# Optimization experiments

Hardware: AMD Instinct MI355X
Metric: run time of the kernel (lower is better)

The kernel has to match this reference:

```python
import jax, jax.numpy as jnp
import numpy as np

D_STATE = 8
DT_RANK = 16
D_CONV = 4


def layernorm(x, w, b, eps=1e-5):
    mu = jnp.mean(x, axis=-1, keepdims=True)
    var = jnp.var(x, axis=-1, keepdims=True)
    return (x - mu) * jax.lax.rsqrt(var + eps) * w + b


def silu(x):
    return x * jax.nn.sigmoid(x)


def dwconv_causal(x, w, b):
    # x: [B,L,D], w: [D,K] depthwise causal conv (mamba conv1d, padding=K-1 then truncate)
    K = w.shape[1]
    xp = jnp.pad(x, ((0, 0), (K - 1, 0), (0, 0)))
    y = jax.lax.conv_general_dilated(
        xp, w.T[:, None, :], (1,), 'VALID',
        dimension_numbers=('NWC', 'WIO', 'NWC'),
        feature_group_count=w.shape[0])
    return y + b


def selective_scan(u, dt, A, Bm, Cm, Dp):
    # u, dt: [b,l,d]; A: [d,n]; Bm, Cm: [b,l,n]; Dp: [d]
    def step(h, inp):
        dt_t, B_t, C_t, u_t = inp           # [b,d],[b,n],[b,n],[b,d]
        dA = jnp.exp(dt_t[..., None] * A)   # [b,d,n]
        h = dA * h + dt_t[..., None] * B_t[:, None, :] * u_t[..., None]
        y = jnp.einsum('bdn,bn->bd', h, C_t)
        return h, y
    b, l, d = u.shape
    h0 = jnp.zeros((b, d, A.shape[1]), u.dtype)
    xs = (dt.transpose(1, 0, 2), Bm.transpose(1, 0, 2),
          Cm.transpose(1, 0, 2), u.transpose(1, 0, 2))
    _, ys = jax.lax.scan(step, h0, xs)
    return ys.transpose(1, 0, 2) + u * Dp


def scan_dir(x, xe, cw, cb, cew, ceb, xpw, dtw, dtb, A_log, Dp):
    # one scan direction: u from x (input0 path), dt/B/C from xe (extra_emb path)
    xc = silu(dwconv_causal(x, cw, cb))
    ec = silu(dwconv_causal(xe, cew, ceb))
    dbl = ec @ xpw.T                                   # [b,l,dt_rank+2n]
    dtr = dbl[..., :DT_RANK]
    Bm = dbl[..., DT_RANK:DT_RANK + D_STATE]
    Cm = dbl[..., DT_RANK + D_STATE:]
    dt = jax.nn.softplus(dtr @ dtw.T + dtb)
    A = -jnp.exp(A_log)
    return selective_scan(xc, dt, A, Bm, Cm, Dp)


def forward(input0, input1, norm0_w, norm0_b, norm1_w, norm1_b,
            in_proj_w, in_proj_extra_w,
            convx_w, convx_b, conve_w, conve_b,
            convx_w_r, convx_b_r, conve_w_r, conve_b_r,
            xproj_w, xproj_w_r, dtproj_w, dtproj_b, dtproj_w_r, dtproj_b_r,
            A_log, A_log_r, Dp, Dp_r, outnorm_w, outnorm_b, outproj_w):
    skip = input0
    h0 = layernorm(input0, norm0_w, norm0_b)
    h1 = layernorm(input1, norm1_w, norm1_b)
    xz = h0 @ in_proj_w.T                     # [b,l,2d]
    d = in_proj_w.shape[0] // 2
    x, z = xz[..., :d], xz[..., d:]
    xe = h1 @ in_proj_extra_w.T               # [b,l,d]
    # forward-direction scan
    y_f = scan_dir(x, xe, convx_w, convx_b, conve_w, conve_b,
                   xproj_w, dtproj_w, dtproj_b, A_log, Dp)
    # backward-direction scan (flip sequence, scan, flip back)
    xr, xer = jnp.flip(x, 1), jnp.flip(xe, 1)
    y_b = scan_dir(xr, xer, convx_w_r, convx_b_r, conve_w_r, conve_b_r,
                   xproj_w_r, dtproj_w_r, dtproj_b_r, A_log_r, Dp_r)
    y = (y_f + jnp.flip(y_b, 1)) * 0.5        # if_devide_out=True
    y = layernorm(y, outnorm_w, outnorm_b)    # use_norm=True
    y = y * silu(z)
    out = y @ outproj_w.T
    return out + skip


def setup_inputs() -> dict:
    key = jax.random.key(0)
    B, H, W, dim = 2, 128, 128, 256
    L, d, n, dtr, K = H * W, dim, D_STATE, DT_RANK, D_CONV
    ks = jax.random.split(key, 24)
    s = 0.02
    inp = {
        'input0': jax.random.normal(ks[0], (B, L, dim), jnp.float32),
        'input1': jax.random.normal(ks[1], (B, L, dim), jnp.float32),
        'norm0_w': jnp.ones((dim,), jnp.float32),
        'norm0_b': jnp.zeros((dim,), jnp.float32),
        'norm1_w': jnp.ones((dim,), jnp.float32),
        'norm1_b': jnp.zeros((dim,), jnp.float32),
        'in_proj_w': jax.random.normal(ks[2], (2 * d, dim), jnp.float32) * s,
        'in_proj_extra_w': jax.random.normal(ks[3], (d, dim), jnp.float32) * s,
        'convx_w': jax.random.normal(ks[4], (d, K), jnp.float32) * 0.2,
        'convx_b': jnp.zeros((d,), jnp.float32),
        'conve_w': jax.random.normal(ks[5], (d, K), jnp.float32) * 0.2,
        'conve_b': jnp.zeros((d,), jnp.float32),
        'convx_w_r': jax.random.normal(ks[6], (d, K), jnp.float32) * 0.2,
        'convx_b_r': jnp.zeros((d,), jnp.float32),
        'conve_w_r': jax.random.normal(ks[7], (d, K), jnp.float32) * 0.2,
        'conve_b_r': jnp.zeros((d,), jnp.float32),
        'xproj_w': jax.random.normal(ks[8], (dtr + 2 * n, d), jnp.float32) * s,
        'xproj_w_r': jax.random.normal(ks[9], (dtr + 2 * n, d), jnp.float32) * s,
        'dtproj_w': jax.random.normal(ks[10], (d, dtr), jnp.float32) * 0.1,
        'dtproj_b': jax.random.uniform(ks[11], (d,), jnp.float32, -4.0, -2.0),
        'dtproj_w_r': jax.random.normal(ks[12], (d, dtr), jnp.float32) * 0.1,
        'dtproj_b_r': jax.random.uniform(ks[13], (d,), jnp.float32, -4.0, -2.0),
        'A_log': jnp.tile(jnp.log(jnp.arange(1, n + 1, dtype=jnp.float32)), (d, 1)),
        'A_log_r': jnp.tile(jnp.log(jnp.arange(1, n + 1, dtype=jnp.float32)), (d, 1)),
        'Dp': jnp.ones((d,), jnp.float32),
        'Dp_r': jnp.ones((d,), jnp.float32),
        'outnorm_w': jnp.ones((d,), jnp.float32),
        'outnorm_b': jnp.zeros((d,), jnp.float32),
        'outproj_w': jax.random.normal(ks[14], (dim, d), jnp.float32) * s,
    }
    return inp


def reference(input0, input1, norm0_w, norm0_b, norm1_w, norm1_b,
              in_proj_w, in_proj_extra_w,
              convx_w, convx_b, conve_w, conve_b,
              convx_w_r, convx_b_r, conve_w_r, conve_b_r,
              xproj_w, xproj_w_r, dtproj_w, dtproj_b, dtproj_w_r, dtproj_b_r,
              A_log, A_log_r, Dp, Dp_r, outnorm_w, outnorm_b, outproj_w):
    return forward(input0, input1, norm0_w, norm0_b, norm1_w, norm1_b,
                   in_proj_w, in_proj_extra_w,
                   convx_w, convx_b, conve_w, conve_b,
                   convx_w_r, convx_b_r, conve_w_r, conve_b_r,
                   xproj_w, xproj_w_r, dtproj_w, dtproj_b, dtproj_w_r, dtproj_b_r,
                   A_log, A_log_r, Dp, Dp_r, outnorm_w, outnorm_b, outproj_w)
```

## Files before the change

kernel.cpp:

```cpp
#include <hip/hip_runtime.h>
#include <math.h>

#define L_SEQ 16384
#define DIM 256
#define NST 8
#define RNK 16
#define S_TOT 32768
#define NCH 512
#define CLH 32

typedef __attribute__((ext_vector_type(8))) short bf16x8;
typedef __attribute__((ext_vector_type(4))) float f32x4;

__device__ __forceinline__ float bf2f(unsigned short u) {
  union { unsigned int i; float f; } v; v.i = ((unsigned int)u) << 16; return v.f;
}
__device__ __forceinline__ unsigned short f2bf(float x) {
  union { float f; unsigned int i; } v; v.f = x;
  unsigned int r = v.i + 0x7fffu + ((v.i >> 16) & 1u);
  return (unsigned short)(r >> 16);
}
__device__ __forceinline__ float rcpf(float x) {
  return __builtin_amdgcn_rcpf(x);
}

__global__ __launch_bounds__(256) void ln_norm(
    const float* __restrict__ in0, const float* __restrict__ in1,
    const float* __restrict__ w0, const float* __restrict__ b0,
    const float* __restrict__ w1, const float* __restrict__ b1,
    unsigned short* __restrict__ h0, unsigned short* __restrict__ h1,
    const float* __restrict__ pw0, const float* __restrict__ pw1,
    const float* __restrict__ pw2, unsigned short* __restrict__ wbout) {
  int which = blockIdx.y;
  if (which == 0 && blockIdx.x < 1024) {
    int i = blockIdx.x * 256 + threadIdx.x;
    if (i < 131072) wbout[i] = f2bf(pw0[i]);
    else if (i < 196608) wbout[i] = f2bf(pw1[i - 131072]);
    else wbout[i] = f2bf(pw2[i - 196608]);
  }
  int row = blockIdx.x * 4 + (threadIdx.x >> 6);
  int lane = threadIdx.x & 63;
  const float* x = (which ? in1 : in0) + (size_t)row * DIM;
  const float* w = which ? w1 : w0;
  const float* b = which ? b1 : b0;
  unsigned short* h = which ? h1 : h0;
  float4 v = *(const float4*)&x[lane * 4];
  float s = v.x + v.y + v.z + v.w;
  float s2 = v.x * v.x + v.y * v.y + v.z * v.z + v.w * v.w;
  for (int off = 32; off; off >>= 1) {
    s += __shfl_xor(s, off);
    s2 += __shfl_xor(s2, off);
  }
  float mean = s * (1.0f / DIM);
  float var = s2 * (1.0f / DIM) - mean * mean;
  float rstd = rsqrtf(var + 1e-5f);
  float4 wv = *(const float4*)&w[lane * 4];
  float4 bv = *(const float4*)&b[lane * 4];
  ushort4 out;
  out.x = f2bf((v.x - mean) * rstd * wv.x + bv.x);
  out.y = f2bf((v.y - mean) * rstd * wv.y + bv.y);
  out.z = f2bf((v.z - mean) * rstd * wv.z + bv.z);
  out.w = f2bf((v.w - mean) * rstd * wv.w + bv.w);
  *(ushort4*)&h[(size_t)row * DIM + lane * 4] = out;
}

template <int BF16C, int ADDIN>
__global__ __launch_bounds__(256) void gemm64(
    const unsigned short* __restrict__ A, int lda,
    const unsigned short* __restrict__ Wb,
    void* __restrict__ Cv, const float* __restrict__ addp, int Nn) {
  __shared__ unsigned short As[64 * 256];
  __shared__ unsigned short Ws[64 * 256];
  int tid = threadIdx.x;
  int n0 = blockIdx.x * 64, m0 = blockIdx.y * 64;
  for (int i = 0; i < 8; ++i) {
    int f8 = tid + i * 256;
    int r = f8 >> 5, c8 = (f8 & 31) * 8;
    int sc = c8 ^ ((r & 7) << 3);
    *(uint4*)&As[r * 256 + sc] = *(const uint4*)&A[(size_t)(m0 + r) * lda + c8];
    *(uint4*)&Ws[r * 256 + sc] = *(const uint4*)&Wb[(size_t)(n0 + r) * 256 + c8];
  }
  __syncthreads();
  int wid = tid >> 6, lane = tid & 63;
  int wm = wid >> 1, wn = wid & 1;
  int l15 = lane & 15, lk = (lane >> 4) * 8;
  f32x4 acc[2][2] = {};
  for (int ks = 0; ks < 8; ++ks) {
    int kcol = ks * 32 + lk;
    bf16x8 af[2], bf_[2];
    for (int mf = 0; mf < 2; ++mf) {
      int row = wm * 32 + mf * 16 + l15;
      af[mf] = *(const bf16x8*)&As[row * 256 + (kcol ^ ((row & 7) << 3))];
    }
    for (int nf = 0; nf < 2; ++nf) {
      int row = wn * 32 + nf * 16 + l15;
      bf_[nf] = *(const bf16x8*)&Ws[row * 256 + (kcol ^ ((row & 7) << 3))];
    }
    for (int mf = 0; mf < 2; ++mf)
      for (int nf = 0; nf < 2; ++nf)
        acc[mf][nf] = __builtin_amdgcn_mfma_f32_16x16x32_bf16(
            af[mf], bf_[nf], acc[mf][nf], 0, 0, 0);
  }
  for (int mf = 0; mf < 2; ++mf)
    for (int nf = 0; nf < 2; ++nf) {
      int row = m0 + wm * 32 + mf * 16 + (lane >> 4) * 4;
      int col = n0 + wn * 32 + nf * 16 + l15;
      for (int v = 0; v < 4; ++v) {
        size_t off = (size_t)(row + v) * Nn + col;
        float val = acc[mf][nf][v];
        if (ADDIN) val += addp[off];
        if (BF16C) ((unsigned short*)Cv)[off] = f2bf(val);
        else       ((float*)Cv)[off] = val;
      }
    }
}

__global__ __launch_bounds__(256) void gemm_in(
    const unsigned short* __restrict__ h0, const unsigned short* __restrict__ h1,
    const unsigned short* __restrict__ wb_in, const unsigned short* __restrict__ wb_ex,
    unsigned short* __restrict__ xzOut, unsigned short* __restrict__ xeOut) {
  __shared__ unsigned short As[64 * 256];
  __shared__ unsigned short Ws[64 * 256];
  int tid = threadIdx.x;
  bool isX = blockIdx.x >= 4;
  const unsigned short* A = isX ? h0 : h1;
  const unsigned short* Wb = isX ? wb_in : wb_ex;
  unsigned short* Cv = isX ? xzOut : xeOut;
  int Nn = isX ? 512 : 256;
  int n0 = (isX ? (int)blockIdx.x - 4 : (int)blockIdx.x) * 64;
  int m0 = blockIdx.y * 64;
  for (int i = 0; i < 8; ++i) {
    int f8 = tid + i * 256;
    int r = f8 >> 5, c8 = (f8 & 31) * 8;
    int sc = c8 ^ ((r & 7) << 3);
    *(uint4*)&As[r * 256 + sc] = *(const uint4*)&A[(size_t)(m0 + r) * 256 + c8];
    *(uint4*)&Ws[r * 256 + sc] = *(const uint4*)&Wb[(size_t)(n0 + r) * 256 + c8];
  }
  __syncthreads();
  int wid = tid >> 6, lane = tid & 63;
  int wm = wid >> 1, wn = wid & 1;
  int l15 = lane & 15, lk = (lane >> 4) * 8;
  f32x4 acc[2][2] = {};
  for (int ks = 0; ks < 8; ++ks) {
    int kcol = ks * 32 + lk;
    bf16x8 af[2], bf_[2];
    for (int mf = 0; mf < 2; ++mf) {
      int row = wm * 32 + mf * 16 + l15;
      af[mf] = *(const bf16x8*)&As[row * 256 + (kcol ^ ((row & 7) << 3))];
    }
    for (int nf = 0; nf < 2; ++nf) {
      int row = wn * 32 + nf * 16 + l15;
      bf_[nf] = *(const bf16x8*)&Ws[row * 256 + (kcol ^ ((row & 7) << 3))];
    }
    for (int mf = 0; mf < 2; ++mf)
      for (int nf = 0; nf < 2; ++nf)
        acc[mf][nf] = __builtin_amdgcn_mfma_f32_16x16x32_bf16(
            af[mf], bf_[nf], acc[mf][nf], 0, 0, 0);
  }
  for (int mf = 0; mf < 2; ++mf)
    for (int nf = 0; nf < 2; ++nf) {
      int row = m0 + wm * 32 + mf * 16 + (lane >> 4) * 4;
      int col = n0 + wn * 32 + nf * 16 + l15;
      for (int v = 0; v < 4; ++v) {
        size_t off = (size_t)(row + v) * Nn + col;
        Cv[off] = f2bf(acc[mf][nf][v]);
      }
    }
}

__global__ __launch_bounds__(256) void gemm_out_fused(
    const unsigned short* __restrict__ ycomb,
    const unsigned short* __restrict__ ybu,
    const unsigned short* __restrict__ xz,
    const float* __restrict__ onw, const float* __restrict__ onb,
    const unsigned short* __restrict__ Wb,
    float* __restrict__ outp, const float* __restrict__ addp) {
  __shared__ unsigned short As[64 * 256];
  __shared__ unsigned short Ws[64 * 256];
  __shared__ float muS[64], rsS[64];
  int tid = threadIdx.x;
  int n0 = blockIdx.x * 64, m0 = blockIdx.y * 64;
  for (int i = 0; i < 8; ++i) {
    int f8 = tid + i * 256;
    int r = f8 >> 5, c8 = (f8 & 31) * 8;
    int sc = c8 ^ ((r & 7) << 3);
    *(uint4*)&Ws[r * 256 + sc] = *(const uint4*)&Wb[(size_t)(n0 + r) * 256 + c8];
    int m = m0 + r;
    int b = m >> 14, l = m & (L_SEQ - 1);
    const unsigned short* pf = &ycomb[(size_t)m * DIM + c8];
    const unsigned short* pb =
        &ybu[((size_t)S_TOT + ((size_t)b << 14) + (L_SEQ - 1 - l)) * DIM + c8];
    ushort4 f0 = *(const ushort4*)pf, f1 = *(const ushort4*)(pf + 4);
    ushort4 b0 = *(const ushort4*)pb, b1 = *(const ushort4*)(pb + 4);
    float v[8];
    v[0] = 0.5f * (bf2f(f0.x) + bf2f(b0.x));
    v[1] = 0.5f * (bf2f(f0.y) + bf2f(b0.y));
    v[2] = 0.5f * (bf2f(f0.z) + bf2f(b0.z));
    v[3] = 0.5f * (bf2f(f0.w) + bf2f(b0.w));
    v[4] = 0.5f * (bf2f(f1.x) + bf2f(b1.x));
    v[5] = 0.5f * (bf2f(f1.y) + bf2f(b1.y));
    v[6] = 0.5f * (bf2f(f1.z) + bf2f(b1.z));
    v[7] = 0.5f * (bf2f(f1.w) + bf2f(b1.w));
    float s = 0.f, s2 = 0.f;
    for (int j = 0; j < 8; ++j) { s += v[j]; s2 += v[j] * v[j]; }
    for (int off = 16; off; off >>= 1) {
      s += __shfl_xor(s, off);
      s2 += __shfl_xor(s2, off);
    }
    if ((tid & 31) == 0) {
      float mean = s * (1.0f / DIM);
      float var = s2 * (1.0f / DIM) - mean * mean;
      muS[r] = mean;
      rsS[r] = rsqrtf(var + 1e-5f);
    }
    uint4 pk;
    pk.x = (unsigned int)f2bf(v[0]) | ((unsigned int)f2bf(v[1]) << 16);
    pk.y = (unsigned int)f2bf(v[2]) | ((unsigned int)f2bf(v[3]) << 16);
    pk.z = (unsigned int)f2bf(v[4]) | ((unsigned int)f2bf(v[5]) << 16);
    pk.w = (unsigned int)f2bf(v[6]) | ((unsigned int)f2bf(v[7]) << 16);
    *(uint4*)&As[r * 256 + sc] = pk;
  }
  __syncthreads();
  for (int i = 0; i < 8; ++i) {
    int f8 = tid + i * 256;
    int r = f8 >> 5, c8 = (f8 & 31) * 8;
    int sc = c8 ^ ((r & 7) << 3);
    int m = m0 + r;
    uint4 pk = *(const uint4*)&As[r * 256 + sc];
    float v[8];
    v[0] = bf2f((unsigned short)(pk.x & 0xffff));
    v[1] = bf2f((unsigned short)(pk.x >> 16));
    v[2] = bf2f((unsigned short)(pk.y & 0xffff));
    v[3] = bf2f((unsigned short)(pk.y >> 16));
    v[4] = bf2f((unsigned short)(pk.z & 0xffff));
    v[5] = bf2f((unsigned short)(pk.z >> 16));
    v[6] = bf2f((unsigned short)(pk.w & 0xffff));
    v[7] = bf2f((unsigned short)(pk.w >> 16));
    const unsigned short* pz = &xz[(size_t)m * 512 + 256 + c8];
    ushort4 z0 = *(const ushort4*)pz, z1 = *(const ushort4*)(pz + 4);
    float zf[8] = {bf2f(z0.x), bf2f(z0.y), bf2f(z0.z), bf2f(z0.w),
                   bf2f(z1.x), bf2f(z1.y), bf2f(z1.z), bf2f(z1.w)};
    float4 w0 = *(const float4*)&onw[c8];
    float4 w1 = *(const float4*)&onw[c8 + 4];
    float4 bb0 = *(const float4*)&onb[c8];
    float4 bb1 = *(const float4*)&onb[c8 + 4];
    float wv[8] = {w0.x, w0.y, w0.z, w0.w, w1.x, w1.y, w1.z, w1.w};
    float bv[8] = {bb0.x, bb0.y, bb0.z, bb0.w, bb1.x, bb1.y, bb1.z, bb1.w};
    float mean = muS[r], rstd = rsS[r];
    unsigned int o[4];
    for (int jj = 0; jj < 4; ++jj) {
      int j0 = jj * 2, j1 = jj * 2 + 1;
      float ln0 = (v[j0] - mean) * rstd * wv[j0] + bv[j0];
      float ln1 = (v[j1] - mean) * rstd * wv[j1] + bv[j1];
      float g0 = ln0 * (zf[j0] * rcpf(1.f + __expf(-zf[j0])));
      float g1 = ln1 * (zf[j1] * rcpf(1.f + __expf(-zf[j1])));
      o[jj] = (unsigned int)f2bf(g0) | ((unsigned int)f2bf(g1) << 16);
    }
    uint4 w4; w4.x = o[0]; w4.y = o[1]; w4.z = o[2]; w4.w = o[3];
    *(uint4*)&As[r * 256 + sc] = w4;
  }
  __syncthreads();
  int wid = tid >> 6, lane = tid & 63;
  int wm = wid >> 1, wn = wid & 1;
  int l15 = lane & 15, lk = (lane >> 4) * 8;
  f32x4 acc[2][2] = {};
  for (int ks = 0; ks < 8; ++ks) {
    int kcol = ks * 32 + lk;
    bf16x8 af[2], bf_[2];
    for (int mf = 0; mf < 2; ++mf) {
      int row = wm * 32 + mf * 16 + l15;
      af[mf] = *(const bf16x8*)&As[row * 256 + (kcol ^ ((row & 7) << 3))];
    }
    for (int nf = 0; nf < 2; ++nf) {
      int row = wn * 32 + nf * 16 + l15;
      bf_[nf] = *(const bf16x8*)&Ws[row * 256 + (kcol ^ ((row & 7) << 3))];
    }
    for (int mf = 0; mf < 2; ++mf)
      for (int nf = 0; nf < 2; ++nf)
        acc[mf][nf] = __builtin_amdgcn_mfma_f32_16x16x32_bf16(
            af[mf], bf_[nf], acc[mf][nf], 0, 0, 0);
  }
  for (int mf = 0; mf < 2; ++mf)
    for (int nf = 0; nf < 2; ++nf) {
      int row = m0 + wm * 32 + mf * 16 + (lane >> 4) * 4;
      int col = n0 + wn * 32 + nf * 16 + l15;
      for (int v = 0; v < 4; ++v) {
        size_t off = (size_t)(row + v) * 256 + col;
        outp[off] = acc[mf][nf][v] + addp[off];
      }
    }
}

__global__ __launch_bounds__(256) void xproj_mfma(
    const unsigned short* __restrict__ xe,
    const float* __restrict__ conve_w, const float* __restrict__ conve_b,
    const float* __restrict__ conve_w_r, const float* __restrict__ conve_b_r,
    const float* __restrict__ xproj_w, const float* __restrict__ xproj_w_r,
    unsigned short* __restrict__ dbl2) {
  __shared__ unsigned short ecS[64 * 256];
  __shared__ unsigned short xwS[32 * 256];
  int chunk = blockIdx.x;
  int dir = blockIdx.y;
  int b = chunk >> 8;
  int t0 = (chunk & 255) * 64;
  int tid = threadIdx.x;
  const float* cw = dir ? conve_w_r : conve_w;
  const float* cb = dir ? conve_b_r : conve_b;
  const float* xw = dir ? xproj_w_r : xproj_w;

  for (int i = tid; i < 32 * 256; i += 256) {
    int o = i >> 8, dd = i & 255;
    xwS[o * 256 + (((dd & ~7) ^ ((o & 7) << 3)) | (dd & 7))] = f2bf(xw[i]);
  }

  {
    int c = tid;
    float w0 = cw[c * 4 + 0], w1 = cw[c * 4 + 1], w2 = cw[c * 4 + 2],
          w3 = cw[c * 4 + 3], bias = cb[c];
    size_t bL = (size_t)b * L_SEQ;
    auto loadx = [&](int t) -> float {
      if (t < 0) return 0.f;
      int src = dir ? (L_SEQ - 1 - t) : t;
      return bf2f(xe[(bL + src) * DIM + c]);
    };
    float xm3 = loadx(t0 - 3), xm2 = loadx(t0 - 2), xm1 = loadx(t0 - 1);
    const unsigned short* xp =
        &xe[(bL + (dir ? (L_SEQ - 1 - t0) : t0)) * DIM + c];
    int xstep = dir ? -DIM : DIM;
    int cbase = c & ~7, clow = c & 7;
    for (int t4 = 0; t4 < 64; t4 += 4) {
      float xin4[4];
      for (int j = 0; j < 4; ++j) xin4[j] = bf2f(xp[(ptrdiff_t)j * xstep]);
      xp += (ptrdiff_t)4 * xstep;
      for (int j = 0; j < 4; ++j) {
        int tl = t4 + j;
        float xin = xin4[j];
        float pre = w0 * xm3 + w1 * xm2 + w2 * xm1 + w3 * xin + bias;
        float u = pre * rcpf(1.f + __expf(-pre));
        xm3 = xm2; xm2 = xm1; xm1 = xin;
        ecS[tl * 256 + ((cbase ^ ((tl & 7) << 3)) | clow)] = f2bf(u);
      }
    }
  }
  __syncthreads();

  int wid = tid >> 6, lane = tid & 63;
  int l15 = lane & 15, lk = (lane >> 4) * 8;
  f32x4 acc[2] = {};
  for (int kk = 0; kk < 8; ++kk) {
    int kcol = kk * 32 + lk;
    int row = wid * 16 + l15;
    bf16x8 af = *(const bf16x8*)&ecS[row * 256 + (kcol ^ ((row & 7) << 3))];
    for (int ni = 0; ni < 2; ++ni) {
      int o = ni * 16 + l15;
      bf16x8 bfr = *(const bf16x8*)&xwS[o * 256 + (kcol ^ ((o & 7) << 3))];
      acc[ni] = __builtin_amdgcn_mfma_f32_16x16x32_bf16(af, bfr, acc[ni], 0, 0, 0);
    }
  }
  size_t mbase = (size_t)dir * S_TOT + (size_t)chunk * 64;
  int rloc = wid * 16 + (lane >> 4) * 4;
  for (int ni = 0; ni < 2; ++ni) {
    int o = ni * 16 + l15;
    for (int v = 0; v < 4; ++v)
      dbl2[(mbase + rloc + v) * 32 + o] = f2bf(acc[ni][v]);
  }
}

__global__ __launch_bounds__(256) void dtu_compute(
    const unsigned short* __restrict__ dbl2,
    const float* __restrict__ dtw, const float* __restrict__ dtw_r,
    const float* __restrict__ dtb, const float* __restrict__ dtb_r,
    unsigned short* __restrict__ dt_arr,
    const unsigned short* __restrict__ xz,
    const float* __restrict__ convx_w, const float* __restrict__ convx_b,
    const float* __restrict__ convx_w_r, const float* __restrict__ convx_b_r,
    unsigned short* __restrict__ u_arr) {
  __shared__ unsigned short dtwS[256 * 32];
  __shared__ unsigned short dtrS[64 * 32];
  __shared__ unsigned short outS[64 * 256];
  int tid = threadIdx.x;
  if (blockIdx.x < 1024) {
    int m0 = blockIdx.x * 64;
    int dir = (blockIdx.x >= 512) ? 1 : 0;
    const float* dw = dir ? dtw_r : dtw;
    const float* db = dir ? dtb_r : dtb;
    {
      uint4 z; z.x = 0; z.y = 0; z.z = 0; z.w = 0;
      for (int i = tid; i < 1280; i += 256) {
        if (i < 1024) ((uint4*)dtwS)[i] = z;
        else          ((uint4*)dtrS)[i - 1024] = z;
      }
    }
    __syncthreads();
    for (int it = 0; it < 4; ++it) {
      int idx = tid + it * 256;
      int c = idx >> 2, k4 = idx & 3;
      float4 v = *(const float4*)&dw[c * 16 + k4 * 4];
      uint2 pk;
      pk.x = (unsigned int)f2bf(v.x) | ((unsigned int)f2bf(v.y) << 16);
      pk.y = (unsigned int)f2bf(v.z) | ((unsigned int)f2bf(v.w) << 16);
      int byte = c * 64 + (((k4 >> 1) ^ (c & 3)) << 4) + ((k4 & 1) << 3);
      *(uint2*)((char*)dtwS + byte) = pk;
    }
    {
      int r = tid >> 2, k4 = tid & 3;
      uint2 pk = *(const uint2*)&dbl2[(size_t)(m0 + r) * 32 + k4 * 4];
      int byte = r * 64 + (((k4 >> 1) ^ (r & 3)) << 4) + ((k4 & 1) << 3);
      *(uint2*)((char*)dtrS + byte) = pk;
    }
    __syncthreads();
    int wid = tid >> 6, lane = tid & 63;
    int l15 = lane & 15, lkc = lane >> 4;
    bf16x8 af[4];
    for (int mi = 0; mi < 4; ++mi) {
      int r = mi * 16 + l15;
      af[mi] = *(const bf16x8*)((char*)dtrS + r * 64 + ((lkc ^ (r & 3)) << 4));
    }
    f32x4 acc[4][4] = {};
    for (int ni = 0; ni < 4; ++ni) {
      int c = (wid * 4 + ni) * 16 + l15;
      bf16x8 bfr = *(const bf16x8*)((char*)dtwS + c * 64 + ((lkc ^ (c & 3)) << 4));
      for (int mi = 0; mi < 4; ++mi)
        acc[mi][ni] = __builtin_amdgcn_mfma_f32_16x16x32_bf16(
            af[mi], bfr, acc[mi][ni], 0, 0, 0);
    }
    for (int ni = 0; ni < 4; ++ni) {
      int c = (wid * 4 + ni) * 16 + l15;
      float bias_ = db[c];
      int cb_ = c & ~7, cl_ = c & 7;
      for (int mi = 0; mi < 4; ++mi) {
        int rb = mi * 16 + (lane >> 4) * 4;
        for (int v = 0; v < 4; ++v) {
          int r = rb + v;
          float xdt = acc[mi][ni][v] + bias_;
          float dtv = (xdt > 15.f) ? xdt : __logf(1.f + __expf(xdt));
          outS[r * 256 + ((cb_ ^ ((r & 7) << 3)) | cl_)] = f2bf(dtv);
        }
      }
    }
    __syncthreads();
    for (int it = 0; it < 8; ++it) {
      int i = tid + it * 256;
      int r = i >> 5, cg = (i & 31) * 8;
      uint4 val = *(const uint4*)&outS[r * 256 + (cg ^ ((r & 7) << 3))];
      *(uint4*)&dt_arr[(size_t)(m0 + r) * 256 + cg] = val;
    }
  } else {
    int chunk = blockIdx.x - 1024;
    int b = chunk >> 9;
    int t0 = (chunk & 511) * 32;
    int c = tid;
    float w0 = convx_w[c * 4 + 0], w1 = convx_w[c * 4 + 1],
          w2 = convx_w[c * 4 + 2], w3 = convx_w[c * 4 + 3], bias = convx_b[c];
    float w0r = convx_w_r[c * 4 + 0], w1r = convx_w_r[c * 4 + 1],
          w2r = convx_w_r[c * 4 + 2], w3r = convx_w_r[c * 4 + 3],
          biasr = convx_b_r[c];
    size_t bL = (size_t)b * L_SEQ;
    auto ld = [&](int t) -> float {
      if (t < 0 || t >= L_SEQ) return 0.f;
      return bf2f(xz[(bL + t) * 512 + c]);
    };
    float x3 = ld(t0 - 3), x2 = ld(t0 - 2), x1 = ld(t0 - 1);
    unsigned short* op0 = &u_arr[(bL + t0) * DIM + c];
    unsigned short* op1 =
        &u_arr[((size_t)S_TOT + bL + (L_SEQ - 1 - t0)) * DIM + c];
    for (int tg = 0; tg < 36; tg += 4) {
      float xin4[4];
      for (int j = 0; j < 4; ++j) xin4[j] = ld(t0 + tg + j);
      for (int j = 0; j < 4; ++j) {
        int tl = tg + j;
        float xin = xin4[j];
        if (tl < 32) {
          float pre = w0 * x3 + w1 * x2 + w2 * x1 + w3 * xin + bias;
          op0[(size_t)tl * DIM] = f2bf(pre * rcpf(1.f + __expf(-pre)));
        }
        if (tl >= 3 && tl < 35) {
          float prer = w0r * xin + w1r * x1 + w2r * x2 + w3r * x3 + biasr;
          int s = tl - 3;
          *(op1 - (ptrdiff_t)s * DIM) = f2bf(prer * rcpf(1.f + __expf(-prer)));
        }
        x3 = x2; x2 = x1; x1 = xin;
      }
    }
  }
}

#define DA8(FASTA)                                                    \
  float dA[NST];                                                      \
  if (FASTA) {                                                        \
    float e1 = __expf(-dtv);                                          \
    dA[0] = e1;                                                       \
    for (int n = 1; n < NST; ++n) dA[n] = dA[n - 1] * e1;             \
  } else {                                                            \
    for (int n = 0; n < NST; ++n) dA[n] = __expf(dtv * Ar[n]);        \
  }

template <int USE_UDT>
__global__ __launch_bounds__(256) void scan_pass1(
    const unsigned short* __restrict__ xz, const unsigned short* __restrict__ dbl2,
    const unsigned short* __restrict__ u_arr,
    const unsigned short* __restrict__ dt_arr,
    const float* __restrict__ convx_w, const float* __restrict__ convx_b,
    const float* __restrict__ convx_w_r, const float* __restrict__ convx_b_r,
    const float* __restrict__ dtproj_w, const float* __restrict__ dtproj_b,
    const float* __restrict__ dtproj_w_r, const float* __restrict__ dtproj_b_r,
    const float* __restrict__ A_log, const float* __restrict__ A_log_r,
    float* __restrict__ Pc, float* __restrict__ Qc) {
  int chunk = blockIdx.x, b = blockIdx.y, dir = blockIdx.z;
  int d = threadIdx.x;
  const float* al = dir ? A_log_r : A_log;
  float w0 = 0.f, w1 = 0.f, w2 = 0.f, w3 = 0.f, bias = 0.f, dbias = 0.f;
  float dwreg[RNK];
  if (!USE_UDT) {
    const float* cw = dir ? convx_w_r : convx_w;
    const float* cb = dir ? convx_b_r : convx_b;
    const float* dw = dir ? dtproj_w_r : dtproj_w;
    const float* dbp = dir ? dtproj_b_r : dtproj_b;
    w0 = cw[d * 4 + 0]; w1 = cw[d * 4 + 1]; w2 = cw[d * 4 + 2];
    w3 = cw[d * 4 + 3]; bias = cb[d]; dbias = dbp[d];
    for (int r = 0; r < RNK; ++r) dwreg[r] = dw[d * RNK + r];
  }
  float Ar[NST];
  bool fa = true;
  for (int n = 0; n < NST; ++n) {
    Ar[n] = -__expf(al[d * NST + n]);
    fa = fa && (fabsf(Ar[n] + (float)(n + 1)) < 1e-4f * (float)(n + 1));
  }
  bool fastA = (__ballot(fa) == ~0ULL);

  __shared__ float dblS[CLH][32];
  int t0 = chunk * CLH;
  size_t dtbase = (size_t)dir * S_TOT + (size_t)b * L_SEQ;
  if (USE_UDT) {
    int i = d;
    dblS[i >> 3][i & 7] =
        bf2f(dbl2[(dtbase + t0 + (i >> 3)) * 32 + 16 + (i & 7)]);
  } else {
    for (int i = d; i < CLH * 32; i += 256)
      dblS[i >> 5][i & 31] = bf2f(dbl2[(dtbase + t0) * 32 + i]);
  }
  __syncthreads();
  auto loadx = [&](int t) -> float {
    if (t < 0) return 0.f;
    int srct = dir ? (L_SEQ - 1 - t) : t;
    return bf2f(xz[((size_t)b * L_SEQ + srct) * 512 + d]);
  };
  float xm3 = 0.f, xm2 = 0.f, xm1 = 0.f;
  if (!USE_UDT) { xm3 = loadx(t0 - 3); xm2 = loadx(t0 - 2); xm1 = loadx(t0 - 1); }
  const unsigned short* up = &u_arr[(dtbase + t0) * DIM + d];
  const unsigned short* dtp = &dt_arr[(dtbase + t0) * DIM + d];
  float Q[NST];
  for (int n = 0; n < NST; ++n) Q[n] = 0.f;
  float sdt = 0.f;
  const int BOFF = USE_UDT ? 0 : 16;

#define P1_GRP(FASTA)                                                      \
  for (int t8 = 0; t8 < CLH; t8 += 8) {                                    \
    float uu[8], dd[8];                                                    \
    for (int j = 0; j < 8; ++j) {                                          \
      uu[j] = bf2f(up[(size_t)j * DIM]);                                   \
      dd[j] = bf2f(dtp[(size_t)j * DIM]);                                  \
    }                                                                      \
    up += 8 * DIM; dtp += 8 * DIM;                                         \
    for (int j = 0; j < 8; ++j) {                                          \
      const float* row = dblS[t8 + j];                                     \
      float u = uu[j], dtv = dd[j];                                        \
      float du = dtv * u;                                                  \
      sdt += dtv;                                                          \
      DA8(FASTA)                                                           \
      float4 B0 = *(const float4*)(row);                                   \
      float4 B1 = *(const float4*)(row + 4);                               \
      Q[0] = dA[0] * Q[0] + du * B0.x; Q[1] = dA[1] * Q[1] + du * B0.y;    \
      Q[2] = dA[2] * Q[2] + du * B0.z; Q[3] = dA[3] * Q[3] + du * B0.w;    \
      Q[4] = dA[4] * Q[4] + du * B1.x; Q[5] = dA[5] * Q[5] + du * B1.y;    \
      Q[6] = dA[6] * Q[6] + du * B1.z; Q[7] = dA[7] * Q[7] + du * B1.w;    \
    }                                                                      \
  }

#define P1_STEP(FASTA)                                                     \
  {                                                                        \
    const float* row = dblS[tl];                                           \
    float u, dtv;                                                          \
    {                                                                      \
      float xin = loadx(t0 + tl);                                          \
      float pre = w0 * xm3 + w1 * xm2 + w2 * xm1 + w3 * xin + bias;        \
      u = pre * rcpf(1.f + __expf(-pre));                                  \
      xm3 = xm2; xm2 = xm1; xm1 = xin;                                     \
      float4 q0 = *(const float4*)(row);                                   \
      float4 q1 = *(const float4*)(row + 4);                               \
      float4 q2 = *(const float4*)(row + 8);                               \
      float4 q3 = *(const float4*)(row + 12);                              \
      float xdt = dbias + q0.x * dwreg[0] + q0.y * dwreg[1] +              \
                  q0.z * dwreg[2] + q0.w * dwreg[3] + q1.x * dwreg[4] +    \
                  q1.y * dwreg[5] + q1.z * dwreg[6] + q1.w * dwreg[7] +    \
                  q2.x * dwreg[8] + q2.y * dwreg[9] + q2.z * dwreg[10] +   \
                  q2.w * dwreg[11] + q3.x * dwreg[12] + q3.y * dwreg[13] + \
                  q3.z * dwreg[14] + q3.w * dwreg[15];                     \
      dtv = (xdt > 15.f) ? xdt : __logf(1.f + __expf(xdt));                \
    }                                                                      \
    float du = dtv * u;                                                    \
    sdt += dtv;                                                            \
    DA8(FASTA)                                                             \
    float4 B0 = *(const float4*)(row + BOFF);                              \
    float4 B1 = *(const float4*)(row + BOFF + 4);                          \
    Q[0] = dA[0] * Q[0] + du * B0.x; Q[1] = dA[1] * Q[1] + du * B0.y;      \
    Q[2] = dA[2] * Q[2] + du * B0.z; Q[3] = dA[3] * Q[3] + du * B0.w;      \
    Q[4] = dA[4] * Q[4] + du * B1.x; Q[5] = dA[5] * Q[5] + du * B1.y;      \
    Q[6] = dA[6] * Q[6] + du * B1.z; Q[7] = dA[7] * Q[7] + du * B1.w;      \
  }

  if (USE_UDT) {
    if (fastA) { P1_GRP(1) } else { P1_GRP(0) }
  } else {
    if (fastA) {
      for (int tl = 0; tl < CLH; ++tl) P1_STEP(1)
    } else {
      for (int tl = 0; tl < CLH; ++tl) P1_STEP(0)
    }
  }
#undef P1_STEP
#undef P1_GRP

  float P[NST];
  if (fastA) {
    float E = __expf(-sdt);
    P[0] = E;
    for (int n = 1; n < NST; ++n) P[n] = P[n - 1] * E;
  } else {
    for (int n = 0; n < NST; ++n) P[n] = __expf(Ar[n] * sdt);
  }
  size_t obase = ((((size_t)(dir * 2 + b)) * NCH + chunk) * DIM + d) * NST;
  for (int n = 0; n < NST; ++n) { Pc[obase + n] = P[n]; Qc[obase + n] = Q[n]; }
}

__global__ __launch_bounds__(256) void scan_mid(
    float* __restrict__ Pc, const float* __restrict__ Qc) {
  int idx = blockIdx.x * 256 + threadIdx.x;
  int dn = idx & 2047;
  int db_ = idx >> 11;
  size_t base = (size_t)db_ * NCH * 2048 + dn;
  float h = 0.f;
  for (int c0 = 0; c0 < NCH; c0 += 8) {
    size_t off = base + (size_t)c0 * 2048;
    float P[8], Q[8];
#pragma unroll
    for (int j = 0; j < 8; ++j) {
      P[j] = Pc[off + (size_t)j * 2048];
      Q[j] = Qc[off + (size_t)j * 2048];
    }
#pragma unroll
    for (int j = 0; j < 8; ++j) {
      Pc[off + (size_t)j * 2048] = h;
      h = P[j] * h + Q[j];
    }
  }
}

template <int MODE>
__global__ __launch_bounds__(256) void scan_pass2(
    const unsigned short* __restrict__ xz, const unsigned short* __restrict__ dbl2,
    unsigned short* __restrict__ u_arr,
    const unsigned short* __restrict__ dt_arr,
    const float* __restrict__ convx_w, const float* __restrict__ convx_b,
    const float* __restrict__ convx_w_r, const float* __restrict__ convx_b_r,
    const float* __restrict__ dtproj_w, const float* __restrict__ dtproj_b,
    const float* __restrict__ dtproj_w_r, const float* __restrict__ dtproj_b_r,
    const float* __restrict__ A_log, const float* __restrict__ A_log_r,
    const float* __restrict__ Dp, const float* __restrict__ Dp_r,
    const float* __restrict__ Hinit, unsigned short* __restrict__ ycomb,
    int dirParam) {
  int chunk = blockIdx.x, b = blockIdx.y;
  int dir = MODE ? blockIdx.z : dirParam;
  int d = threadIdx.x;
  const float* al = dir ? A_log_r : A_log;
  float Dv = (dir ? Dp_r : Dp)[d];
  float w0 = 0.f, w1 = 0.f, w2 = 0.f, w3 = 0.f, bias = 0.f, dbias = 0.f;
  float dwreg[RNK];
  if (!MODE) {
    const float* cw = dir ? convx_w_r : convx_w;
    const float* cb = dir ? convx_b_r : convx_b;
    const float* dw = dir ? dtproj_w_r : dtproj_w;
    const float* dbp = dir ? dtproj_b_r : dtproj_b;
    w0 = cw[d * 4 + 0]; w1 = cw[d * 4 + 1]; w2 = cw[d * 4 + 2];
    w3 = cw[d * 4 + 3]; bias = cb[d];
    dbias = dbp[d];
    for (int r = 0; r < RNK; ++r) dwreg[r] = dw[d * RNK + r];
  }
  float Ar[NST];
  bool fa = true;
  for (int n = 0; n < NST; ++n) {
    Ar[n] = -__expf(al[d * NST + n]);
    fa = fa && (fabsf(Ar[n] + (float)(n + 1)) < 1e-4f * (float)(n + 1));
  }
  bool fastA = (__ballot(fa) == ~0ULL);

  __shared__ float dblS[CLH][32];
  int t0 = chunk * CLH;
  size_t dtbase = (size_t)dir * S_TOT + (size_t)b * L_SEQ;
  if (MODE) {
    for (int i = d; i < CLH * 16; i += 256)
      dblS[i >> 4][i & 15] =
          bf2f(dbl2[(dtbase + t0 + (i >> 4)) * 32 + 16 + (i & 15)]);
  } else {
    for (int i = d; i < CLH * 32; i += 256)
      dblS[i >> 5][i & 31] = bf2f(dbl2[(dtbase + t0) * 32 + i]);
  }
  __syncthreads();
  auto loadx = [&](int t) -> float {
    if (t < 0) return 0.f;
    int srct = dir ? (L_SEQ - 1 - t) : t;
    return bf2f(xz[((size_t)b * L_SEQ + srct) * 512 + d]);
  };
  float xm3 = 0.f, xm2 = 0.f, xm1 = 0.f;
  if (!MODE) { xm3 = loadx(t0 - 3); xm2 = loadx(t0 - 2); xm1 = loadx(t0 - 1); }
  float h[NST];
  size_t hbase = ((((size_t)(dir * 2 + b)) * NCH + chunk) * DIM + d) * NST;
  for (int n = 0; n < NST; ++n) h[n] = Hinit[hbase + n];
  unsigned short* up = &u_arr[(dtbase + t0) * DIM + d];
  const unsigned short* dtp = &dt_arr[(dtbase + t0) * DIM + d];
  unsigned short* yc = &ycomb[((size_t)b * L_SEQ + t0) * DIM + d];

#define P2_GRP(FASTA)                                                      \
  for (int t8 = 0; t8 < CLH; t8 += 8) {                                    \
    float uu[8], dd[8];                                                    \
    for (int j = 0; j < 8; ++j) {                                          \
      uu[j] = bf2f(up[(size_t)j * DIM]);                                   \
      dd[j] = bf2f(dtp[(size_t)j * DIM]);                                  \
    }                                                                      \
    for (int j = 0; j < 8; ++j) {                                          \
      const float* row = dblS[t8 + j];                                     \
      float u = uu[j], dtv = dd[j];                                        \
      float du = dtv * u;                                                  \
      DA8(FASTA)                                                           \
      float4 B0 = *(const float4*)(row);                                   \
      float4 B1 = *(const float4*)(row + 4);                               \
      float4 C0 = *(const float4*)(row + 8);                               \
      float4 C1 = *(const float4*)(row + 12);                              \
      h[0] = dA[0] * h[0] + du * B0.x; h[1] = dA[1] * h[1] + du * B0.y;    \
      h[2] = dA[2] * h[2] + du * B0.z; h[3] = dA[3] * h[3] + du * B0.w;    \
      h[4] = dA[4] * h[4] + du * B1.x; h[5] = dA[5] * h[5] + du * B1.y;    \
      h[6] = dA[6] * h[6] + du * B1.z; h[7] = dA[7] * h[7] + du * B1.w;    \
      float y = C0.x * h[0] + C0.y * h[1] + C0.z * h[2] + C0.w * h[3] +    \
                C1.x * h[4] + C1.y * h[5] + C1.z * h[6] + C1.w * h[7] +    \
                u * Dv;                                                    \
      if (dir == 0) yc[(size_t)j * DIM] = f2bf(y);                         \
      else          up[(size_t)j * DIM] = f2bf(y);                         \
    }                                                                      \
    up += 8 * DIM; dtp += 8 * DIM; yc += 8 * DIM;                          \
  }

#define P2_STEP(FASTA)                                                     \
  {                                                                        \
    int t = t0 + tl;                                                       \
    const float* row = dblS[tl];                                           \
    float u, dtv;                                                          \
    {                                                                      \
      float xin = loadx(t);                                                \
      float pre = w0 * xm3 + w1 * xm2 + w2 * xm1 + w3 * xin + bias;        \
      u = pre * rcpf(1.f + __expf(-pre));                                  \
      xm3 = xm2; xm2 = xm1; xm1 = xin;                                     \
      float4 q0 = *(const float4*)(row);                                   \
      float4 q1 = *(const float4*)(row + 4);                               \
      float4 q2 = *(const float4*)(row + 8);                               \
      float4 q3 = *(const float4*)(row + 12);                              \
      float xdt = dbias + q0.x * dwreg[0] + q0.y * dwreg[1] +              \
                  q0.z * dwreg[2] + q0.w * dwreg[3] + q1.x * dwreg[4] +    \
                  q1.y * dwreg[5] + q1.z * dwreg[6] + q1.w * dwreg[7] +    \
                  q2.x * dwreg[8] + q2.y * dwreg[9] + q2.z * dwreg[10] +   \
                  q2.w * dwreg[11] + q3.x * dwreg[12] + q3.y * dwreg[13] + \
                  q3.z * dwreg[14] + q3.w * dwreg[15];                     \
      dtv = (xdt > 15.f) ? xdt : __logf(1.f + __expf(xdt));                \
    }                                                                      \
    float du = dtv * u;                                                    \
    DA8(FASTA)                                                             \
    float4 B0 = *(const float4*)(row + 16);                                \
    float4 B1 = *(const float4*)(row + 20);                                \
    float4 C0 = *(const float4*)(row + 24);                                \
    float4 C1 = *(const float4*)(row + 28);                                \
    h[0] = dA[0] * h[0] + du * B0.x; h[1] = dA[1] * h[1] + du * B0.y;      \
    h[2] = dA[2] * h[2] + du * B0.z; h[3] = dA[3] * h[3] + du * B0.w;      \
    h[4] = dA[4] * h[4] + du * B1.x; h[5] = dA[5] * h[5] + du * B1.y;      \
    h[6] = dA[6] * h[6] + du * B1.z; h[7] = dA[7] * h[7] + du * B1.w;      \
    float y = C0.x * h[0] + C0.y * h[1] + C0.z * h[2] + C0.w * h[3] +      \
              C1.x * h[4] + C1.y * h[5] + C1.z * h[6] + C1.w * h[7] +      \
              u * Dv;                                                      \
    if (dir == 0) {                                                        \
      ycomb[((size_t)b * L_SEQ + t) * DIM + d] = f2bf(y);                  \
    } else {                                                               \
      size_t o = ((size_t)b * L_SEQ + (L_SEQ - 1 - t)) * DIM + d;          \
      float prev = bf2f(ycomb[o]);                                         \
      ycomb[o] = f2bf(0.5f * (prev + y));                                  \
    }                                                                      \
  }

  if (MODE) {
    if (fastA) { P2_GRP(1) } else { P2_GRP(0) }
  } else {
    if (fastA) {
      for (int tl = 0; tl < CLH; ++tl) P2_STEP(1)
    } else {
      for (int tl = 0; tl < CLH; ++tl) P2_STEP(0)
    }
  }
#undef P2_STEP
#undef P2_GRP
}

__global__ __launch_bounds__(256) void combine_ln(
    const unsigned short* __restrict__ ycomb,
    unsigned short* __restrict__ xz,
    const float* __restrict__ onw, const float* __restrict__ onb) {
  int m = blockIdx.x * 4 + (threadIdx.x >> 6);
  int lane = threadIdx.x & 63;
  ushort4 y4 = *(const ushort4*)&ycomb[(size_t)m * DIM + lane * 4];
  float v0 = bf2f(y4.x), v1 = bf2f(y4.y), v2 = bf2f(y4.z), v3 = bf2f(y4.w);
  float s = v0 + v1 + v2 + v3;
  float s2 = v0 * v0 + v1 * v1 + v2 * v2 + v3 * v3;
  for (int off = 32; off; off >>= 1) {
    s += __shfl_xor(s, off);
    s2 += __shfl_xor(s2, off);
  }
  float mean = s * (1.0f / DIM);
  float var = s2 * (1.0f / DIM) - mean * mean;
  float rstd = rsqrtf(var + 1e-5f);
  ushort4 z4 = *(const ushort4*)&xz[(size_t)m * 512 + 256 + lane * 4];
  float zf[4] = {bf2f(z4.x), bf2f(z4.y), bf2f(z4.z), bf2f(z4.w)};
  float vf[4] = {v0, v1, v2, v3};
  ushort4 out;
  unsigned short* op = (unsigned short*)&out;
  for (int j = 0; j < 4; ++j) {
    int c = lane * 4 + j;
    float ln = (vf[j] - mean) * rstd * onw[c] + onb[c];
    op[j] = f2bf(ln * (zf[j] * rcpf(1.f + __expf(-zf[j]))));
  }
  *(ushort4*)&xz[(size_t)m * 512 + lane * 4] = out;
}

extern "C" void kernel_launch(void* const* d_in, const int* in_sizes, int n_in,
                              void* d_out, int out_size, void* d_ws, size_t ws_size,
                              hipStream_t stream) {
  const float* input0 = (const float*)d_in[0];
  const float* input1 = (const float*)d_in[1];
  const float* norm0_w = (const float*)d_in[2];
  const float* norm0_b = (const float*)d_in[3];
  const float* norm1_w = (const float*)d_in[4];
  const float* norm1_b = (const float*)d_in[5];
  const float* in_proj_w = (const float*)d_in[6];
  const float* in_proj_extra_w = (const float*)d_in[7];
  const float* convx_w = (const float*)d_in[8];
  const float* convx_b = (const float*)d_in[9];
  const float* conve_w = (const float*)d_in[10];
  const float* conve_b = (const float*)d_in[11];
  const float* convx_w_r = (const float*)d_in[12];
  const float* convx_b_r = (const float*)d_in[13];
  const float* conve_w_r = (const float*)d_in[14];
  const float* conve_b_r = (const float*)d_in[15];
  const float* xproj_w = (const float*)d_in[16];
  const float* xproj_w_r = (const float*)d_in[17];
  const float* dtproj_w = (const float*)d_in[18];
  const float* dtproj_b = (const float*)d_in[19];
  const float* dtproj_w_r = (const float*)d_in[20];
  const float* dtproj_b_r = (const float*)d_in[21];
  const float* A_log = (const float*)d_in[22];
  const float* A_log_r = (const float*)d_in[23];
  const float* Dp = (const float*)d_in[24];
  const float* Dp_r = (const float*)d_in[25];
  const float* outnorm_w = (const float*)d_in[26];
  const float* outnorm_b = (const float*)d_in[27];
  const float* outproj_w = (const float*)d_in[28];

  char* w = (char*)d_ws;
  unsigned short* xz    = (unsigned short*)(w + 0);
  unsigned short* h0    = (unsigned short*)(w + 33554432);
  unsigned short* ycomb = (unsigned short*)(w + 33554432);
  float* Qc   = (float*)(w + 33554432);
  unsigned short* xe    = (unsigned short*)(w + 50331648);
  float* Pc   = (float*)(w + 50331648);
  unsigned short* dbl2 = (unsigned short*)(w + 67108864);
  unsigned short* wb = (unsigned short*)(w + 75497472);
  unsigned short* wb_in  = wb;
  unsigned short* wb_ex  = wb + 131072;
  unsigned short* wb_out = wb + 196608;
  unsigned short* u_arr  = (unsigned short*)(w + 76021760);
  unsigned short* dt_arr = (unsigned short*)(w + 109576192);
  const bool big = ws_size >= 76021760ULL + 67108864ULL;
  unsigned short* h1 = big ? u_arr : xz;

  ln_norm<<<dim3(S_TOT / 4, 2), 256, 0, stream>>>(
      input0, input1, norm0_w, norm0_b, norm1_w, norm1_b, h0, h1,
      in_proj_w, in_proj_extra_w, outproj_w, wb);
  if (big) {
    gemm_in<<<dim3(12, 512), 256, 0, stream>>>(h0, h1, wb_in, wb_ex, xz, xe);
  } else {
    gemm64<1, 0><<<dim3(4, 512), 256, 0, stream>>>(h1, DIM, wb_ex, xe, nullptr, 256);
    gemm64<1, 0><<<dim3(8, 512), 256, 0, stream>>>(h0, DIM, wb_in, xz, nullptr, 512);
  }
  xproj_mfma<<<dim3(512, 2), 256, 0, stream>>>(
      xe, conve_w, conve_b, conve_w_r, conve_b_r, xproj_w, xproj_w_r, dbl2);
  if (big) {
    dtu_compute<<<dim3(2048), 256, 0, stream>>>(
        dbl2, dtproj_w, dtproj_w_r, dtproj_b, dtproj_b_r, dt_arr,
        xz, convx_w, convx_b, convx_w_r, convx_b_r, u_arr);
    scan_pass1<1><<<dim3(NCH, 2, 2), 256, 0, stream>>>(
        xz, dbl2, u_arr, dt_arr, convx_w, convx_b, convx_w_r, convx_b_r,
        dtproj_w, dtproj_b, dtproj_w_r, dtproj_b_r, A_log, A_log_r, Pc, Qc);
  } else {
    scan_pass1<0><<<dim3(NCH, 2, 2), 256, 0, stream>>>(
        xz, dbl2, u_arr, dt_arr, convx_w, convx_b, convx_w_r, convx_b_r,
        dtproj_w, dtproj_b, dtproj_w_r, dtproj_b_r, A_log, A_log_r, Pc, Qc);
  }
  scan_mid<<<dim3(32), 256, 0, stream>>>(Pc, Qc);
  if (big) {
    scan_pass2<1><<<dim3(NCH, 2, 2), 256, 0, stream>>>(
        xz, dbl2, u_arr, dt_arr, convx_w, convx_b, convx_w_r, convx_b_r,
        dtproj_w, dtproj_b, dtproj_w_r, dtproj_b_r, A_log, A_log_r,
        Dp, Dp_r, Pc, ycomb, 0);
    gemm_out_fused<<<dim3(4, 512), 256, 0, stream>>>(
        ycomb, u_arr, xz, outnorm_w, outnorm_b, wb_out, (float*)d_out, input0);
  } else {
    for (int dir = 0; dir < 2; ++dir)
      scan_pass2<0><<<dim3(NCH, 2), 256, 0, stream>>>(
          xz, dbl2, u_arr, dt_arr, convx_w, convx_b, convx_w_r, convx_b_r,
          dtproj_w, dtproj_b, dtproj_w_r, dtproj_b_r, A_log, A_log_r,
          Dp, Dp_r, Pc, ycomb, dir);
    combine_ln<<<dim3(S_TOT / 4), 256, 0, stream>>>(ycomb, xz, outnorm_w, outnorm_b);
    gemm64<0, 1><<<dim3(4, 512), 256, 0, stream>>>(
        xz, 512, wb_out, d_out, input0, 256);
  }
}
```

Before: 237.8 us.

## Loop over N tiles inside GEMM blocks to reuse A tile and prologue

The input-projection and output-projection GEMMs now give each block one 64-row A tile and loop over all N tiles, streaming weight tiles through shared memory, instead of launching one block per (M,N) tile. The A tile is loaded once per block. In the output GEMM the combine, LayerNorm and gating prologue runs once per row block rather than once per N tile, and its two-phase shared-memory pass is replaced by per-thread statistics computed in registers. The trade-off is fewer blocks (1024 and 512), each running a serial N loop with a barrier per tile, so there is less parallelism and no overlap between the weight load and the MFMA work.

```diff
diff --git a/kernel.cpp b/kernel.cpp
--- a/kernel.cpp
+++ b/kernel.cpp
@@ -115,60 +115,69 @@
     }
 }
 
-__global__ __launch_bounds__(256) void gemm_in(
+__global__ __launch_bounds__(256) void gemm_in2(
     const unsigned short* __restrict__ h0, const unsigned short* __restrict__ h1,
     const unsigned short* __restrict__ wb_in, const unsigned short* __restrict__ wb_ex,
     unsigned short* __restrict__ xzOut, unsigned short* __restrict__ xeOut) {
   __shared__ unsigned short As[64 * 256];
   __shared__ unsigned short Ws[64 * 256];
   int tid = threadIdx.x;
-  bool isX = blockIdx.x >= 4;
+  bool isX = blockIdx.x < 512;
   const unsigned short* A = isX ? h0 : h1;
   const unsigned short* Wb = isX ? wb_in : wb_ex;
   unsigned short* Cv = isX ? xzOut : xeOut;
   int Nn = isX ? 512 : 256;
-  int n0 = (isX ? (int)blockIdx.x - 4 : (int)blockIdx.x) * 64;
-  int m0 = blockIdx.y * 64;
+  int NT = isX ? 8 : 4;
+  int m0 = (isX ? (int)blockIdx.x : (int)blockIdx.x - 512) * 64;
   for (int i = 0; i < 8; ++i) {
     int f8 = tid + i * 256;
     int r = f8 >> 5, c8 = (f8 & 31) * 8;
     int sc = c8 ^ ((r & 7) << 3);
     *(uint4*)&As[r * 256 + sc] = *(const uint4*)&A[(size_t)(m0 + r) * 256 + c8];
-    *(uint4*)&Ws[r * 256 + sc] = *(const uint4*)&Wb[(size_t)(n0 + r) * 256 + c8];
-  }
-  __syncthreads();
+  }
   int wid = tid >> 6, lane = tid & 63;
   int wm = wid >> 1, wn = wid & 1;
   int l15 = lane & 15, lk = (lane >> 4) * 8;
-  f32x4 acc[2][2] = {};
-  for (int ks = 0; ks < 8; ++ks) {
-    int kcol = ks * 32 + lk;
-    bf16x8 af[2], bf_[2];
-    for (int mf = 0; mf < 2; ++mf) {
-      int row = wm * 32 + mf * 16 + l15;
-      af[mf] = *(const bf16x8*)&As[row * 256 + (kcol ^ ((row & 7) << 3))];
-    }
-    for (int nf = 0; nf < 2; ++nf) {
-      int row = wn * 32 + nf * 16 + l15;
-      bf_[nf] = *(const bf16x8*)&Ws[row * 256 + (kcol ^ ((row & 7) << 3))];
+  for (int nt = 0; nt < NT; ++nt) {
+    int n0 = nt * 64;
+    for (int i = 0; i < 8; ++i) {
+      int f8 = tid + i * 256;
+      int r = f8 >> 5, c8 = (f8 & 31) * 8;
+      int sc = c8 ^ ((r & 7) << 3);
+      *(uint4*)&Ws[r * 256 + sc] = *(const uint4*)&Wb[(size_t)(n0 + r) * 256 + c8];
+    }
+    __syncthreads();
+    f32x4 acc[2][2] = {};
+    for (int ks = 0; ks < 8; ++ks) {
+      int kcol = ks * 32 + lk;
+      bf16x8 af[2], bf_[2];
+      for (int mf = 0; mf < 2; ++mf) {
+        int row = wm * 32 + mf * 16 + l15;
+        af[mf] = *(const bf16x8*)&As[row * 256 + (kcol ^ ((row & 7) << 3))];
+      }
+      for (int nf = 0; nf < 2; ++nf) {
+        int row = wn * 32 + nf * 16 + l15;
+        bf_[nf] = *(const bf16x8*)&Ws[row * 256 + (kcol ^ ((row & 7) << 3))];
+      }
+      for (int mf = 0; mf < 2; ++mf)
+        for (int nf = 0; nf < 2; ++nf)
+          acc[mf][nf] = __builtin_amdgcn_mfma_f32_16x16x32_bf16(
+              af[mf], bf_[nf], acc[mf][nf], 0, 0, 0);
     }
     for (int mf = 0; mf < 2; ++mf)
-      for (int nf = 0; nf < 2; ++nf)
-        acc[mf][nf] = __builtin_amdgcn_mfma_f32_16x16x32_bf16(
-            af[mf], bf_[nf], acc[mf][nf], 0, 0, 0);
-  }
-  for (int mf = 0; mf < 2; ++mf)
-    for (int nf = 0; nf < 2; ++nf) {
-      int row = m0 + wm * 32 + mf * 16 + (lane >> 4) * 4;
-      int col = n0 + wn * 32 + nf * 16 + l15;
-      for (int v = 0; v < 4; ++v) {
-        size_t off = (size_t)(row + v) * Nn + col;
-        Cv[off] = f2bf(acc[mf][nf][v]);
-      }
-    }
-}
-
-__global__ __launch_bounds__(256) void gemm_out_fused(
+      for (int nf = 0; nf < 2; ++nf) {
+        int row = m0 + wm * 32 + mf * 16 + (lane >> 4) * 4;
+        int col = n0 + wn * 32 + nf * 16 + l15;
+        for (int v = 0; v < 4; ++v) {
+          size_t off = (size_t)(row + v) * Nn + col;
+          Cv[off] = f2bf(acc[mf][nf][v]);
+        }
+      }
+    __syncthreads();
+  }
+}
+
+__global__ __launch_bounds__(256) void gemm_out3(
     const unsigned short* __restrict__ ycomb,
     const unsigned short* __restrict__ ybu,
     const unsigned short* __restrict__ xz,
@@ -177,14 +186,12 @@
     float* __restrict__ outp, const float* __restrict__ addp) {
   __shared__ unsigned short As[64 * 256];
   __shared__ unsigned short Ws[64 * 256];
-  __shared__ float muS[64], rsS[64];
   int tid = threadIdx.x;
-  int n0 = blockIdx.x * 64, m0 = blockIdx.y * 64;
+  int m0 = (int)blockIdx.x * 64;
   for (int i = 0; i < 8; ++i) {
     int f8 = tid + i * 256;
     int r = f8 >> 5, c8 = (f8 & 31) * 8;
     int sc = c8 ^ ((r & 7) << 3);
-    *(uint4*)&Ws[r * 256 + sc] = *(const uint4*)&Wb[(size_t)(n0 + r) * 256 + c8];
     int m = m0 + r;
     int b = m >> 14, l = m & (L_SEQ - 1);
     const unsigned short* pf = &ycomb[(size_t)m * DIM + c8];
@@ -207,46 +214,19 @@
       s += __shfl_xor(s, off);
       s2 += __shfl_xor(s2, off);
     }
-    if ((tid & 31) == 0) {
-      float mean = s * (1.0f / DIM);
-      float var = s2 * (1.0f / DIM) - mean * mean;
-      muS[r] = mean;
-      rsS[r] = rsqrtf(var + 1e-5f);
-    }
-    uint4 pk;
-    pk.x = (unsigned int)f2bf(v[0]) | ((unsigned int)f2bf(v[1]) << 16);
-    pk.y = (unsigned int)f2bf(v[2]) | ((unsigned int)f2bf(v[3]) << 16);
-    pk.z = (unsigned int)f2bf(v[4]) | ((unsigned int)f2bf(v[5]) << 16);
-    pk.w = (unsigned int)f2bf(v[6]) | ((unsigned int)f2bf(v[7]) << 16);
-    *(uint4*)&As[r * 256 + sc] = pk;
-  }
-  __syncthreads();
-  for (int i = 0; i < 8; ++i) {
-    int f8 = tid + i * 256;
-    int r = f8 >> 5, c8 = (f8 & 31) * 8;
-    int sc = c8 ^ ((r & 7) << 3);
-    int m = m0 + r;
-    uint4 pk = *(const uint4*)&As[r * 256 + sc];
-    float v[8];
-    v[0] = bf2f((unsigned short)(pk.x & 0xffff));
-    v[1] = bf2f((unsigned short)(pk.x >> 16));
-    v[2] = bf2f((unsigned short)(pk.y & 0xffff));
-    v[3] = bf2f((unsigned short)(pk.y >> 16));
-    v[4] = bf2f((unsigned short)(pk.z & 0xffff));
-    v[5] = bf2f((unsigned short)(pk.z >> 16));
-    v[6] = bf2f((unsigned short)(pk.w & 0xffff));
-    v[7] = bf2f((unsigned short)(pk.w >> 16));
+    float mean = s * (1.0f / DIM);
+    float var = s2 * (1.0f / DIM) - mean * mean;
+    float rstd = rsqrtf(var + 1e-5f);
     const unsigned short* pz = &xz[(size_t)m * 512 + 256 + c8];
     ushort4 z0 = *(const ushort4*)pz, z1 = *(const ushort4*)(pz + 4);
     float zf[8] = {bf2f(z0.x), bf2f(z0.y), bf2f(z0.z), bf2f(z0.w),
                    bf2f(z1.x), bf2f(z1.y), bf2f(z1.z), bf2f(z1.w)};
-    float4 w0 = *(const float4*)&onw[c8];
-    float4 w1 = *(const float4*)&onw[c8 + 4];
+    float4 w0v = *(const float4*)&onw[c8];
+    float4 w1v = *(const float4*)&onw[c8 + 4];
     float4 bb0 = *(const float4*)&onb[c8];
     float4 bb1 = *(const float4*)&onb[c8 + 4];
-    float wv[8] = {w0.x, w0.y, w0.z, w0.w, w1.x, w1.y, w1.z, w1.w};
+    float wv[8] = {w0v.x, w0v.y, w0v.z, w0v.w, w1v.x, w1v.y, w1v.z, w1v.w};
     float bv[8] = {bb0.x, bb0.y, bb0.z, bb0.w, bb1.x, bb1.y, bb1.z, bb1.w};
-    float mean = muS[r], rstd = rsS[r];
     unsigned int o[4];
     for (int jj = 0; jj < 4; ++jj) {
       int j0 = jj * 2, j1 = jj * 2 + 1;
@@ -256,39 +236,49 @@
       float g1 = ln1 * (zf[j1] * rcpf(1.f + __expf(-zf[j1])));
       o[jj] = (unsigned int)f2bf(g0) | ((unsigned int)f2bf(g1) << 16);
     }
-    uint4 w4; w4.x = o[0]; w4.y = o[1]; w4.z = o[2]; w4.w = o[3];
-    *(uint4*)&As[r * 256 + sc] = w4;
-  }
-  __syncthreads();
+    uint4 pk; pk.x = o[0]; pk.y = o[1]; pk.z = o[2]; pk.w = o[3];
+    *(uint4*)&As[r * 256 + sc] = pk;
+  }
   int wid = tid >> 6, lane = tid & 63;
   int wm = wid >> 1, wn = wid & 1;
   int l15 = lane & 15, lk = (lane >> 4) * 8;
-  f32x4 acc[2][2] = {};
-  for (int ks = 0; ks < 8; ++ks) {
-    int kcol = ks * 32 + lk;
-    bf16x8 af[2], bf_[2];
-    for (int mf = 0; mf < 2; ++mf) {
-      int row = wm * 32 + mf * 16 + l15;
-      af[mf] = *(const bf16x8*)&As[row * 256 + (kcol ^ ((row & 7) << 3))];
-    }
-    for (int nf = 0; nf < 2; ++nf) {
-      int row = wn * 32 + nf * 16 + l15;
-      bf_[nf] = *(const bf16x8*)&Ws[row * 256 + (kcol ^ ((row & 7) << 3))];
+  for (int nt = 0; nt < 4; ++nt) {
+    int n0 = nt * 64;
+    for (int i = 0; i < 8; ++i) {
+      int f8 = tid + i * 256;
+      int r = f8 >> 5, c8 = (f8 & 31) * 8;
+      int sc = c8 ^ ((r & 7) << 3);
+      *(uint4*)&Ws[r * 256 + sc] = *(const uint4*)&Wb[(size_t)(n0 + r) * 256 + c8];
+    }
+    __syncthreads();
+    f32x4 acc[2][2] = {};
+    for (int ks = 0; ks < 8; ++ks) {
+      int kcol = ks * 32 + lk;
+      bf16x8 af[2], bf_[2];
+      for (int mf = 0; mf < 2; ++mf) {
+        int row = wm * 32 + mf * 16 + l15;
+        af[mf] = *(const bf16x8*)&As[row * 256 + (kcol ^ ((row & 7) << 3))];
+      }
+      for (int nf = 0; nf < 2; ++nf) {
+        int row = wn * 32 + nf * 16 + l15;
+        bf_[nf] = *(const bf16x8*)&Ws[row * 256 + (kcol ^ ((row & 7) << 3))];
+      }
+      for (int mf = 0; mf < 2; ++mf)
+        for (int nf = 0; nf < 2; ++nf)
+          acc[mf][nf] = __builtin_amdgcn_mfma_f32_16x16x32_bf16(
+              af[mf], bf_[nf], acc[mf][nf], 0, 0, 0);
     }
     for (int mf = 0; mf < 2; ++mf)
-      for (int nf = 0; nf < 2; ++nf)
-        acc[mf][nf] = __builtin_amdgcn_mfma_f32_16x16x32_bf16(
-            af[mf], bf_[nf], acc[mf][nf], 0, 0, 0);
-  }
-  for (int mf = 0; mf < 2; ++mf)
-    for (int nf = 0; nf < 2; ++nf) {
-      int row = m0 + wm * 32 + mf * 16 + (lane >> 4) * 4;
-      int col = n0 + wn * 32 + nf * 16 + l15;
-      for (int v = 0; v < 4; ++v) {
-        size_t off = (size_t)(row + v) * 256 + col;
-        outp[off] = acc[mf][nf][v] + addp[off];
-      }
-    }
+      for (int nf = 0; nf < 2; ++nf) {
+        int row = m0 + wm * 32 + mf * 16 + (lane >> 4) * 4;
+        int col = n0 + wn * 32 + nf * 16 + l15;
+        for (int v = 0; v < 4; ++v) {
+          size_t off = (size_t)(row + v) * 256 + col;
+          outp[off] = acc[mf][nf][v] + addp[off];
+        }
+      }
+    __syncthreads();
+  }
 }
 
 __global__ __launch_bounds__(256) void xproj_mfma(
@@ -890,7 +880,7 @@
       input0, input1, norm0_w, norm0_b, norm1_w, norm1_b, h0, h1,
       in_proj_w, in_proj_extra_w, outproj_w, wb);
   if (big) {
-    gemm_in<<<dim3(12, 512), 256, 0, stream>>>(h0, h1, wb_in, wb_ex, xz, xe);
+    gemm_in2<<<dim3(1024), 256, 0, stream>>>(h0, h1, wb_in, wb_ex, xz, xe);
   } else {
     gemm64<1, 0><<<dim3(4, 512), 256, 0, stream>>>(h1, DIM, wb_ex, xe, nullptr, 256);
     gemm64<1, 0><<<dim3(8, 512), 256, 0, stream>>>(h0, DIM, wb_in, xz, nullptr, 512);
@@ -915,7 +905,7 @@
         xz, dbl2, u_arr, dt_arr, convx_w, convx_b, convx_w_r, convx_b_r,
         dtproj_w, dtproj_b, dtproj_w_r, dtproj_b_r, A_log, A_log_r,
         Dp, Dp_r, Pc, ycomb, 0);
-    gemm_out_fused<<<dim3(4, 512), 256, 0, stream>>>(
+    gemm_out3<<<dim3(512), 256, 0, stream>>>(
         ycomb, u_arr, xz, outnorm_w, outnorm_b, wb_out, (float*)d_out, input0);
   } else {
     for (int dir = 0; dir < 2; ++dir)
```

New measurement: 194.7 us (median of 2 runs). 18.2% less time.
